# Kernel optimization log

Hardware: AMD Instinct MI355X
Metric: run time of the kernel (lower is better)

Reference implementation:

```python
import jax, jax.numpy as jnp
import numpy as np
from jax import lax

KS = 3
N = KS * KS  # 9 sampling points per output pixel


def conv2d(x, w, b, stride=1, pad=1):
    out = lax.conv_general_dilated(
        x, w, (stride, stride), [(pad, pad), (pad, pad)],
        dimension_numbers=("NCHW", "OIHW", "NCHW"))
    return out + b[None, :, None, None]


def setup_inputs() -> dict:
    key = jax.random.key(0)
    k1, k2, k3, k4, k5 = jax.random.split(key, 5)
    inc, outc, b, h, w = 64, 128, 8, 128, 128
    x = jax.random.normal(k1, (b, inc, h, w), jnp.float32)
    # offsets conv: inc -> 3*ks*ks channels, 3x3, pad 1 (small init so offsets are modest)
    off_w = jax.random.normal(k2, (3 * N, inc, 3, 3), jnp.float32) * 0.01
    off_b = jax.random.normal(k3, (3 * N,), jnp.float32) * 0.01
    # main conv: inc -> outc, 3x3, stride=ks, pad 1
    conv_w = jax.random.normal(k4, (outc, inc, 3, 3), jnp.float32) * (1.0 / np.sqrt(inc * 9))
    conv_b = jax.random.normal(k5, (outc,), jnp.float32) * 0.01
    return {"x": x, "off_w": off_w, "off_b": off_b, "conv_w": conv_w, "conv_b": conv_b}


def _deform_forward(x, off_w, off_b, conv_w, conv_b):
    b, c, h, w = x.shape
    ow = conv2d(x, off_w, off_b)               # (b, 3N, h, w)
    offset = ow[:, :2 * N]                      # offset_x (N) then offset_y (N); 3rd chunk (sigmoid
                                                # modulation) is computed in torch but never used.
    # p_0: integer grid coordinates, broadcast over N sampling points
    ii = jnp.arange(h, dtype=x.dtype)
    jj = jnp.arange(w, dtype=x.dtype)
    p0x = jnp.broadcast_to(ii[None, None, :, None], (1, N, h, w))
    p0y = jnp.broadcast_to(jj[None, None, None, :], (1, N, h, w))
    p0 = jnp.concatenate([p0x, p0y], axis=1)    # (1, 2N, h, w)
    p = (p0 + offset).transpose(0, 2, 3, 1)     # (b, h, w, 2N)
    px, py = p[..., :N], p[..., N:]

    q = jnp.floor(p)                            # detached in torch; floor grad is 0 anyway
    qltx = jnp.clip(q[..., :N], 0, h - 1).astype(jnp.int32)
    qlty = jnp.clip(q[..., N:], 0, w - 1).astype(jnp.int32)
    qrbx = jnp.clip(q[..., :N] + 1, 0, h - 1).astype(jnp.int32)
    qrby = jnp.clip(q[..., N:] + 1, 0, w - 1).astype(jnp.int32)

    pxc = jnp.clip(px, 0, h - 1)
    pyc = jnp.clip(py, 0, w - 1)

    xf = x.reshape(b, c, h * w)

    def gather(qx, qy):
        idx = (qx * w + qy).reshape(b, -1)      # (b, h*w*N)
        g = jax.vmap(lambda xb, ib: xb[:, ib])(xf, idx)  # (b, c, h*w*N)
        return g.reshape(b, c, h, w, N)

    f = lambda q_: q_.astype(x.dtype)
    g_lt = (1 + (f(qltx) - pxc)) * (1 + (f(qlty) - pyc))
    g_rb = (1 - (f(qrbx) - pxc)) * (1 - (f(qrby) - pyc))
    g_lb = (1 + (f(qltx) - pxc)) * (1 - (f(qrby) - pyc))
    g_rt = (1 - (f(qrbx) - pxc)) * (1 + (f(qlty) - pyc))

    xo = (g_lt[:, None] * gather(qltx, qlty)
          + g_rb[:, None] * gather(qrbx, qrby)
          + g_lb[:, None] * gather(qltx, qrby)
          + g_rt[:, None] * gather(qrbx, qlty))  # (b, c, h, w, N)

    # rearrange: b c h w (kr kc) -> b c (h kr) (w kc)
    xo = xo.reshape(b, c, h, w, KS, KS).transpose(0, 1, 2, 4, 3, 5).reshape(b, c, h * KS, w * KS)
    return conv2d(xo, conv_w, conv_b, stride=KS, pad=1)  # (b, outc, h, w)


def reference(x, off_w, off_b, conv_w, conv_b):
    return _deform_forward(x, off_w, off_b, conv_w, conv_b)
```

## Files before the change

### kernel.cpp

```cpp
#include <hip/hip_runtime.h>
#include <hip/hip_fp16.h>

#define BB   8
#define CC   64
#define HH   128
#define WW   128
#define OCC  128
#define HWx  (HH*WW)
#define KTOT 576
#define SST  584

typedef __attribute__((ext_vector_type(8))) short short8t;
typedef __attribute__((ext_vector_type(8))) _Float16 half8t;
typedef __attribute__((ext_vector_type(4))) float f32x4;

static __device__ __forceinline__ ushort f2h(float f) {
    __half h = __float2half_rn(f);
    return __half_as_ushort(h);
}

__global__ __launch_bounds__(256) void kfront2(const float* __restrict__ x,
                                               ushort* __restrict__ xTh,
                                               ushort* __restrict__ xTl,
                                               const float* __restrict__ cw,
                                               ushort* __restrict__ wf,
                                               const float* __restrict__ ow,
                                               ushort* __restrict__ woh,
                                               ushort* __restrict__ wol) {
    int bi  = blockIdx.x;
    int tid = threadIdx.x;

    if (bi < 2048) {
        int bb = bi;
        int b  = bb >> 8;
        int p  = (bb & 255) * 64 + (tid & 63);
        int cg = tid >> 6;
        const float* xb = x + (size_t)b * CC * HWx + p;
        size_t base = ((size_t)b * HWx + p) * 64 + cg * 16;
        short8t h0, h1, l0, l1;
#pragma unroll
        for (int e = 0; e < 8; ++e) {
            float v = xb[(size_t)(cg * 16 + e) * HWx];
            __half h = __float2half_rn(v);
            h0[e] = (short)__half_as_ushort(h);
            l0[e] = (short)f2h((v - __half2float(h)) * 2048.f);
        }
#pragma unroll
        for (int e = 0; e < 8; ++e) {
            float v = xb[(size_t)(cg * 16 + 8 + e) * HWx];
            __half h = __float2half_rn(v);
            h1[e] = (short)__half_as_ushort(h);
            l1[e] = (short)f2h((v - __half2float(h)) * 2048.f);
        }
        *(short8t*)(xTh + base)     = h0;
        *(short8t*)(xTh + base + 8) = h1;
        *(short8t*)(xTl + base)     = l0;
        *(short8t*)(xTl + base + 8) = l1;

    } else if (bi < 2336) {
        int i = (bi - 2048) * 256 + tid;
        int e  = i & 7;
        int t  = i >> 3;
        int l  = t & 63;
        int t2 = t >> 6;
        int lr = l & 15, lg = l >> 4;
        int oc = (t2 / 18) * 16 + lr;
        int kg = (t2 % 18) * 32 + lg * 8 + e;
        int c = kg & 63, tap = kg >> 6;
        wf[i] = f2h(cw[oc * 576 + c * 9 + tap]);

    } else {
        int idx = (bi - 2336) * 256 + tid;
        int t   = idx / 18432;
        int r   = idx - t * 18432;
        int nt  = r / 9216;
        int r2  = r - nt * 9216;
        int ks  = r2 / 512;
        int r3  = r2 - ks * 512;
        int l   = r3 >> 3;
        int e   = r3 & 7;
        int k   = ks * 32 + (l >> 4) * 8 + e;
        int tap = k >> 6, c = k & 63;
        int ch  = nt * 16 + (l & 15);
        float val = (ch < 18) ? ow[ch * 576 + c * 9 + tap] * 1024.f : 0.f;
        __half h = __float2half_rn(val);
        if (t == 0) woh[r] = __half_as_ushort(h);
        else        wol[r] = f2h(val - __half2float(h));
    }
}

__global__ __launch_bounds__(256) void koffM(const ushort* __restrict__ xTh,
                                             const ushort* __restrict__ xTl,
                                             const ushort* __restrict__ woh,
                                             const ushort* __restrict__ wol,
                                             const float* __restrict__ off_b,
                                             float* __restrict__ offsT) {
    int tid = threadIdx.x;
    int bi  = blockIdx.x;
    int b   = bi & 7;
    int i   = bi >> 3;
    int wv  = tid >> 6;
    int l   = tid & 63;
    int lr  = l & 15, lg = l >> 4;
    const ushort* xh = xTh + (size_t)b * HWx * 64;
    const ushort* xl = xTl + (size_t)b * HWx * 64;

    f32x4 accA[2][2], accB[2][2];
#pragma unroll
    for (int mt = 0; mt < 2; ++mt)
#pragma unroll
        for (int nt = 0; nt < 2; ++nt)
#pragma unroll
            for (int e = 0; e < 4; ++e) { accA[mt][nt][e] = 0.f; accB[mt][nt][e] = 0.f; }

#pragma unroll
    for (int ks = 0; ks < 18; ++ks) {
        int tap = ks >> 1;
        int di = tap / 3, dj = tap - di * 3;
        int si = i + di - 1;
        bool sv = (si >= 0) && (si < HH);
        int c0 = (ks & 1) * 32 + lg * 8;

        half8t Bh0 = *(const half8t*)(woh + ((0 * 18 + ks) * 64 + l) * 8);
        half8t Bl0 = *(const half8t*)(wol + ((0 * 18 + ks) * 64 + l) * 8);
        half8t Bh1 = *(const half8t*)(woh + ((1 * 18 + ks) * 64 + l) * 8);
        half8t Bl1 = *(const half8t*)(wol + ((1 * 18 + ks) * 64 + l) * 8);

#pragma unroll
        for (int mt = 0; mt < 2; ++mt) {
            int j  = wv * 32 + mt * 16 + lr;
            int sj = j + dj - 1;
            bool v = sv && (sj >= 0) && (sj < WW);
            half8t Ah = {0, 0, 0, 0, 0, 0, 0, 0};
            half8t Al = {0, 0, 0, 0, 0, 0, 0, 0};
            if (v) {
                size_t ao = ((size_t)(si * WW + sj)) * 64 + c0;
                Ah = *(const half8t*)(xh + ao);
                Al = *(const half8t*)(xl + ao);
            }
            accA[mt][0] = __builtin_amdgcn_mfma_f32_16x16x32_f16(Ah, Bh0, accA[mt][0], 0, 0, 0);
            accA[mt][0] = __builtin_amdgcn_mfma_f32_16x16x32_f16(Ah, Bl0, accA[mt][0], 0, 0, 0);
            accB[mt][0] = __builtin_amdgcn_mfma_f32_16x16x32_f16(Al, Bh0, accB[mt][0], 0, 0, 0);
            accA[mt][1] = __builtin_amdgcn_mfma_f32_16x16x32_f16(Ah, Bh1, accA[mt][1], 0, 0, 0);
            accA[mt][1] = __builtin_amdgcn_mfma_f32_16x16x32_f16(Ah, Bl1, accA[mt][1], 0, 0, 0);
            accB[mt][1] = __builtin_amdgcn_mfma_f32_16x16x32_f16(Al, Bh1, accB[mt][1], 0, 0, 0);
        }
    }

    const float sA = 1.f / 1024.f;
    const float sB = 1.f / (1024.f * 2048.f);
#pragma unroll
    for (int mt = 0; mt < 2; ++mt)
#pragma unroll
        for (int nt = 0; nt < 2; ++nt) {
            int ch = nt * 16 + lr;
            if (ch < 18) {
                float bv = off_b[ch];
#pragma unroll
                for (int e = 0; e < 4; ++e) {
                    int pix = wv * 32 + mt * 16 + lg * 4 + e;
                    float val = accA[mt][nt][e] * sA + accB[mt][nt][e] * sB + bv;
                    offsT[((size_t)(b * HWx) + i * WW + pix) * 18 + ch] = val;
                }
            }
        }
}

static __device__ __forceinline__ __half2 lerp_w(uint ltw, uint rbw, uint lbw, uint rtw,
                                                 __half2 hlt, __half2 hrb,
                                                 __half2 hlb, __half2 hrt) {
    __half2 a;
    a = __hmul2(hlt, __builtin_bit_cast(__half2, ltw));
    a = __hfma2(hrb, __builtin_bit_cast(__half2, rbw), a);
    a = __hfma2(hlb, __builtin_bit_cast(__half2, lbw), a);
    a = __hfma2(hrt, __builtin_bit_cast(__half2, rtw), a);
    return a;
}
static __device__ __forceinline__ uint4 lerp_u4(uint4 lt, uint4 rb, uint4 lb, uint4 rt,
                                                __half2 hlt, __half2 hrb,
                                                __half2 hlb, __half2 hrt) {
    uint4 o;
    o.x = __builtin_bit_cast(uint, lerp_w(lt.x, rb.x, lb.x, rt.x, hlt, hrb, hlb, hrt));
    o.y = __builtin_bit_cast(uint, lerp_w(lt.y, rb.y, lb.y, rt.y, hlt, hrb, hlb, hrt));
    o.z = __builtin_bit_cast(uint, lerp_w(lt.z, rb.z, lb.z, rt.z, hlt, hrb, hlb, hrt));
    o.w = __builtin_bit_cast(uint, lerp_w(lt.w, rb.w, lb.w, rt.w, hlt, hrb, hlb, hrt));
    return o;
}

__global__ __launch_bounds__(512, 4) void kmain23(const ushort* __restrict__ xT,
                                                  const float* __restrict__ offsT,
                                                  const ushort* __restrict__ wf,
                                                  const float* __restrict__ conv_b,
                                                  float* __restrict__ out) {
    __shared__ __align__(16) ushort S[32 * SST];
    int tid = threadIdx.x;
    int bi  = blockIdx.x;
    int b   = bi & 7;
    int rem = bi >> 3;
    int oi  = rem >> 2;
    int oj0 = (rem & 3) * 32;

    const ushort* xTb  = xT + (size_t)b * HWx * 64;
    const float*  offb = offsT + (size_t)b * HWx * 18;

    int wv = tid >> 6;
    int l  = tid & 63;
    int lr = l & 15;
    int lg = l >> 4;
    const ushort* wr0 = wf + ((size_t)(wv * 18) * 64 + l) * 8;

#pragma unroll
    for (int it = 0; it < 3; ++it) {
        int s = tid + it * 512;
        if (s >= 1152) break;
        int pix = s / 36;
        int rr  = s - pix * 36;
        int tap = rr >> 2;
        int cg2 = rr & 3;
        int kr = tap / 3, kc = tap - kr * 3;
        int si = oi + ((kr == 0) ? -1 : 0);
        int sj = oj0 + pix + ((kc == 0) ? -1 : 0);
        ushort* Sd = &S[pix * SST + tap * 64 + cg2 * 16];

        if (si < 0 || sj < 0) {
            uint4 z = {0, 0, 0, 0};
            *(uint4*)Sd = z;
            *(uint4*)(Sd + 8) = z;
            continue;
        }
        int n    = ((kr == 0) ? 2 : kr - 1) * 3 + ((kc == 0) ? 2 : kc - 1);
        int pidx = si * WW + sj;
        float ox = offb[pidx * 18 + n];
        float oy = offb[pidx * 18 + 9 + n];
        float px = (float)si + ox;
        float py = (float)sj + oy;
        float fx = floorf(px), fy = floorf(py);
        float pxc   = fminf(fmaxf(px, 0.f), 127.f);
        float pyc   = fminf(fmaxf(py, 0.f), 127.f);
        float qltxf = fminf(fmaxf(fx, 0.f), 127.f);
        float qltyf = fminf(fmaxf(fy, 0.f), 127.f);
        float qrbxf = fminf(fmaxf(fx + 1.f, 0.f), 127.f);
        float qrbyf = fminf(fmaxf(fy + 1.f, 0.f), 127.f);
        int qltx = (int)qltxf, qlty = (int)qltyf;
        int qrbx = (int)qrbxf, qrby = (int)qrbyf;
        int co = cg2 * 16;
        const ushort* plt = xTb + (size_t)(qltx * WW + qlty) * 64 + co;
        const ushort* prb = xTb + (size_t)(qrbx * WW + qrby) * 64 + co;
        const ushort* plb = xTb + (size_t)(qltx * WW + qrby) * 64 + co;
        const ushort* prt = xTb + (size_t)(qrbx * WW + qlty) * 64 + co;
        uint4 lt0 = *(const uint4*)(plt);  uint4 lt1 = *(const uint4*)(plt + 8);
        uint4 rb0 = *(const uint4*)(prb);  uint4 rb1 = *(const uint4*)(prb + 8);
        uint4 lb0 = *(const uint4*)(plb);  uint4 lb1 = *(const uint4*)(plb + 8);
        uint4 rt0 = *(const uint4*)(prt);  uint4 rt1 = *(const uint4*)(prt + 8);

        float glt = (1.f + (qltxf - pxc)) * (1.f + (qltyf - pyc));
        float grb = (1.f - (qrbxf - pxc)) * (1.f - (qrbyf - pyc));
        float glb = (1.f + (qltxf - pxc)) * (1.f - (qrbyf - pyc));
        float grt = (1.f - (qrbxf - pxc)) * (1.f + (qltyf - pyc));
        __half2 hlt = __float2half2_rn(glt);
        __half2 hrb = __float2half2_rn(grb);
        __half2 hlb = __float2half2_rn(glb);
        __half2 hrt = __float2half2_rn(grt);

        uint4 o0 = lerp_u4(lt0, rb0, lb0, rt0, hlt, hrb, hlb, hrt);
        uint4 o1 = lerp_u4(lt1, rb1, lb1, rt1, hlt, hrb, hlb, hrt);
        *(uint4*)(Sd)     = o0;
        *(uint4*)(Sd + 8) = o1;
    }
    __syncthreads();

    f32x4 acc[2];
#pragma unroll
    for (int e = 0; e < 4; ++e) {
        float bv = conv_b[16 * wv + lg * 4 + e];
        acc[0][e] = bv;
        acc[1][e] = bv;
    }
    const ushort* s0 = &S[(lr) * SST + lg * 8];
    const ushort* s1 = &S[(16 + lr) * SST + lg * 8];

#pragma unroll
    for (int ks = 0; ks < 18; ++ks) {
        int kk = ks * 32;
        half8t a0 = *(const half8t*)(wr0 + ks * 512);
        half8t b0 = *(const half8t*)(s0 + kk);
        half8t b1 = *(const half8t*)(s1 + kk);
        acc[0] = __builtin_amdgcn_mfma_f32_16x16x32_f16(a0, b0, acc[0], 0, 0, 0);
        acc[1] = __builtin_amdgcn_mfma_f32_16x16x32_f16(a0, b1, acc[1], 0, 0, 0);
    }

    float* ob = out + ((size_t)b * OCC * HH + oi) * WW + oj0;
#pragma unroll
    for (int p = 0; p < 2; ++p) {
#pragma unroll
        for (int e = 0; e < 4; ++e) {
            int oc  = 16 * wv + lg * 4 + e;
            int col = 16 * p + lr;
            ob[(size_t)oc * HWx + col] = acc[p][e];
        }
    }
}

extern "C" void kernel_launch(void* const* d_in, const int* in_sizes, int n_in,
                              void* d_out, int out_size, void* d_ws, size_t ws_size,
                              hipStream_t stream) {
    const float* x      = (const float*)d_in[0];
    const float* off_w  = (const float*)d_in[1];
    const float* off_b  = (const float*)d_in[2];
    const float* conv_w = (const float*)d_in[3];
    const float* conv_b = (const float*)d_in[4];
    float* out = (float*)d_out;

    char* w0 = (char*)d_ws;
    ushort* wbf   = (ushort*)w0;
    float*  offsT = (float*)(w0 + 147456);
    ushort* xTh   = (ushort*)(w0 + 147456 + 9437184);
    ushort* xTl   = (ushort*)(w0 + 147456 + 9437184 + 16777216);
    ushort* woh   = (ushort*)(w0 + 147456 + 9437184 + 2 * 16777216);
    ushort* wol   = (ushort*)(w0 + 147456 + 9437184 + 2 * 16777216 + 36864);

    kfront2<<<2480, 256, 0, stream>>>(x, xTh, xTl, conv_w, wbf, off_w, woh, wol);
    koffM<<<BB * HH, 256, 0, stream>>>(xTh, xTl, woh, wol, off_b, offsT);
    kmain23<<<BB * HH * 4, 512, 0, stream>>>(xTh, offsT, wbf, conv_b, out);
}
```

Measured before the change: 112.5 us.

## Fuse offset conv into front kernel reading fp32 input directly

The offset convolution now reads the fp32 NCHW input directly and does the hi/lo fp16 split in registers, instead of reading a precomputed transposed xTh/xTl pair. It runs inside the same launch as the xTh transpose and the weight prep. The xTl buffer and its write traffic are removed, and the offset-weight prep moves to a small kernel that runs first. In exchange, the offset conv now does strided, channel-major fp32 loads (eight separate loads per fragment, each a full plane apart) that are less coalesced than the earlier 16-byte vector loads.

```diff
diff --git a/kernel.cpp b/kernel.cpp
--- a/kernel.cpp
+++ b/kernel.cpp
@@ -19,46 +19,128 @@
     return __half_as_ushort(h);
 }
 
-__global__ __launch_bounds__(256) void kfront2(const float* __restrict__ x,
-                                               ushort* __restrict__ xTh,
-                                               ushort* __restrict__ xTl,
-                                               const float* __restrict__ cw,
-                                               ushort* __restrict__ wf,
-                                               const float* __restrict__ ow,
+__global__ __launch_bounds__(256) void kprepw2(const float* __restrict__ ow,
                                                ushort* __restrict__ woh,
                                                ushort* __restrict__ wol) {
+    int idx = blockIdx.x * 256 + threadIdx.x;
+    int t   = idx / 18432;
+    int r   = idx - t * 18432;
+    int nt  = r / 9216;
+    int r2  = r - nt * 9216;
+    int ks  = r2 / 512;
+    int r3  = r2 - ks * 512;
+    int l   = r3 >> 3;
+    int e   = r3 & 7;
+    int k   = ks * 32 + (l >> 4) * 8 + e;
+    int tap = k >> 6, c = k & 63;
+    int ch  = nt * 16 + (l & 15);
+    float val = (ch < 18) ? ow[ch * 576 + c * 9 + tap] * 1024.f : 0.f;
+    __half h = __float2half_rn(val);
+    if (t == 0) woh[r] = __half_as_ushort(h);
+    else        wol[r] = f2h(val - __half2float(h));
+}
+
+__global__ __launch_bounds__(256) void kfront3(const float* __restrict__ x,
+                                               const ushort* __restrict__ woh,
+                                               const ushort* __restrict__ wol,
+                                               const float* __restrict__ off_b,
+                                               float* __restrict__ offsT,
+                                               ushort* __restrict__ xTh,
+                                               const float* __restrict__ cw,
+                                               ushort* __restrict__ wf) {
     int bi  = blockIdx.x;
     int tid = threadIdx.x;
 
-    if (bi < 2048) {
-        int bb = bi;
+    if (bi < 1024) {
+        int b = bi & 7;
+        int i = bi >> 3;
+        int wv = tid >> 6;
+        int l  = tid & 63;
+        int lr = l & 15, lg = l >> 4;
+        const float* xb = x + (size_t)b * CC * HWx;
+
+        f32x4 accA[2][2], accB[2][2];
+#pragma unroll
+        for (int mt = 0; mt < 2; ++mt)
+#pragma unroll
+            for (int nt = 0; nt < 2; ++nt)
+#pragma unroll
+                for (int e = 0; e < 4; ++e) { accA[mt][nt][e] = 0.f; accB[mt][nt][e] = 0.f; }
+
+#pragma unroll
+        for (int ks = 0; ks < 18; ++ks) {
+            int tap = ks >> 1;
+            int di = tap / 3, dj = tap - di * 3;
+            int si = i + di - 1;
+            bool sv = (si >= 0) && (si < HH);
+            int c0 = (ks & 1) * 32 + lg * 8;
+
+            half8t Bh0 = *(const half8t*)(woh + ((0 * 18 + ks) * 64 + l) * 8);
+            half8t Bl0 = *(const half8t*)(wol + ((0 * 18 + ks) * 64 + l) * 8);
+            half8t Bh1 = *(const half8t*)(woh + ((1 * 18 + ks) * 64 + l) * 8);
+            half8t Bl1 = *(const half8t*)(wol + ((1 * 18 + ks) * 64 + l) * 8);
+
+#pragma unroll
+            for (int mt = 0; mt < 2; ++mt) {
+                int j  = wv * 32 + mt * 16 + lr;
+                int sj = j + dj - 1;
+                bool v = sv && (sj >= 0) && (sj < WW);
+                half8t Ah = {0, 0, 0, 0, 0, 0, 0, 0};
+                half8t Al = {0, 0, 0, 0, 0, 0, 0, 0};
+                if (v) {
+                    const float* xp = xb + (size_t)c0 * HWx + si * WW + sj;
+#pragma unroll
+                    for (int e = 0; e < 8; ++e) {
+                        float val = xp[(size_t)e * HWx];
+                        _Float16 h = (_Float16)val;
+                        Ah[e] = h;
+                        Al[e] = (_Float16)((val - (float)h) * 2048.f);
+                    }
+                }
+                accA[mt][0] = __builtin_amdgcn_mfma_f32_16x16x32_f16(Ah, Bh0, accA[mt][0], 0, 0, 0);
+                accA[mt][0] = __builtin_amdgcn_mfma_f32_16x16x32_f16(Ah, Bl0, accA[mt][0], 0, 0, 0);
+                accB[mt][0] = __builtin_amdgcn_mfma_f32_16x16x32_f16(Al, Bh0, accB[mt][0], 0, 0, 0);
+                accA[mt][1] = __builtin_amdgcn_mfma_f32_16x16x32_f16(Ah, Bh1, accA[mt][1], 0, 0, 0);
+                accA[mt][1] = __builtin_amdgcn_mfma_f32_16x16x32_f16(Ah, Bl1, accA[mt][1], 0, 0, 0);
+                accB[mt][1] = __builtin_amdgcn_mfma_f32_16x16x32_f16(Al, Bh1, accB[mt][1], 0, 0, 0);
+            }
+        }
+
+        const float sA = 1.f / 1024.f;
+        const float sB = 1.f / (1024.f * 2048.f);
+#pragma unroll
+        for (int mt = 0; mt < 2; ++mt)
+#pragma unroll
+            for (int nt = 0; nt < 2; ++nt) {
+                int ch = nt * 16 + lr;
+                if (ch < 18) {
+                    float bv = off_b[ch];
+#pragma unroll
+                    for (int e = 0; e < 4; ++e) {
+                        int pix = wv * 32 + mt * 16 + lg * 4 + e;
+                        float val = accA[mt][nt][e] * sA + accB[mt][nt][e] * sB + bv;
+                        offsT[((size_t)(b * HWx) + i * WW + pix) * 18 + ch] = val;
+                    }
+                }
+            }
+
+    } else if (bi < 3072) {
+        int bb = bi - 1024;
         int b  = bb >> 8;
         int p  = (bb & 255) * 64 + (tid & 63);
         int cg = tid >> 6;
         const float* xb = x + (size_t)b * CC * HWx + p;
-        size_t base = ((size_t)b * HWx + p) * 64 + cg * 16;
-        short8t h0, h1, l0, l1;
-#pragma unroll
-        for (int e = 0; e < 8; ++e) {
-            float v = xb[(size_t)(cg * 16 + e) * HWx];
-            __half h = __float2half_rn(v);
-            h0[e] = (short)__half_as_ushort(h);
-            l0[e] = (short)f2h((v - __half2float(h)) * 2048.f);
-        }
-#pragma unroll
-        for (int e = 0; e < 8; ++e) {
-            float v = xb[(size_t)(cg * 16 + 8 + e) * HWx];
-            __half h = __float2half_rn(v);
-            h1[e] = (short)__half_as_ushort(h);
-            l1[e] = (short)f2h((v - __half2float(h)) * 2048.f);
-        }
-        *(short8t*)(xTh + base)     = h0;
-        *(short8t*)(xTh + base + 8) = h1;
-        *(short8t*)(xTl + base)     = l0;
-        *(short8t*)(xTl + base + 8) = l1;
-
-    } else if (bi < 2336) {
-        int i = (bi - 2048) * 256 + tid;
+        ushort* ob = xTh + ((size_t)b * HWx + p) * 64 + cg * 16;
+        short8t v0, v1;
+#pragma unroll
+        for (int e = 0; e < 8; ++e) v0[e] = (short)f2h(xb[(size_t)(cg * 16 + e) * HWx]);
+#pragma unroll
+        for (int e = 0; e < 8; ++e) v1[e] = (short)f2h(xb[(size_t)(cg * 16 + 8 + e) * HWx]);
+        *(short8t*)ob = v0;
+        *(short8t*)(ob + 8) = v1;
+
+    } else {
+        int i = (bi - 3072) * 256 + tid;
         int e  = i & 7;
         int t  = i >> 3;
         int l  = t & 63;
@@ -68,102 +150,7 @@
         int kg = (t2 % 18) * 32 + lg * 8 + e;
         int c = kg & 63, tap = kg >> 6;
         wf[i] = f2h(cw[oc * 576 + c * 9 + tap]);
-
-    } else {
-        int idx = (bi - 2336) * 256 + tid;
-        int t   = idx / 18432;
-        int r   = idx - t * 18432;
-        int nt  = r / 9216;
-        int r2  = r - nt * 9216;
-        int ks  = r2 / 512;
-        int r3  = r2 - ks * 512;
-        int l   = r3 >> 3;
-        int e   = r3 & 7;
-        int k   = ks * 32 + (l >> 4) * 8 + e;
-        int tap = k >> 6, c = k & 63;
-        int ch  = nt * 16 + (l & 15);
-        float val = (ch < 18) ? ow[ch * 576 + c * 9 + tap] * 1024.f : 0.f;
-        __half h = __float2half_rn(val);
-        if (t == 0) woh[r] = __half_as_ushort(h);
-        else        wol[r] = f2h(val - __half2float(h));
-    }
-}
-
-__global__ __launch_bounds__(256) void koffM(const ushort* __restrict__ xTh,
-                                             const ushort* __restrict__ xTl,
-                                             const ushort* __restrict__ woh,
-                                             const ushort* __restrict__ wol,
-                                             const float* __restrict__ off_b,
-                                             float* __restrict__ offsT) {
-    int tid = threadIdx.x;
-    int bi  = blockIdx.x;
-    int b   = bi & 7;
-    int i   = bi >> 3;
-    int wv  = tid >> 6;
-    int l   = tid & 63;
-    int lr  = l & 15, lg = l >> 4;
-    const ushort* xh = xTh + (size_t)b * HWx * 64;
-    const ushort* xl = xTl + (size_t)b * HWx * 64;
-
-    f32x4 accA[2][2], accB[2][2];
-#pragma unroll
-    for (int mt = 0; mt < 2; ++mt)
-#pragma unroll
-        for (int nt = 0; nt < 2; ++nt)
-#pragma unroll
-            for (int e = 0; e < 4; ++e) { accA[mt][nt][e] = 0.f; accB[mt][nt][e] = 0.f; }
-
-#pragma unroll
-    for (int ks = 0; ks < 18; ++ks) {
-        int tap = ks >> 1;
-        int di = tap / 3, dj = tap - di * 3;
-        int si = i + di - 1;
-        bool sv = (si >= 0) && (si < HH);
-        int c0 = (ks & 1) * 32 + lg * 8;
-
-        half8t Bh0 = *(const half8t*)(woh + ((0 * 18 + ks) * 64 + l) * 8);
-        half8t Bl0 = *(const half8t*)(wol + ((0 * 18 + ks) * 64 + l) * 8);
-        half8t Bh1 = *(const half8t*)(woh + ((1 * 18 + ks) * 64 + l) * 8);
-        half8t Bl1 = *(const half8t*)(wol + ((1 * 18 + ks) * 64 + l) * 8);
-
-#pragma unroll
-        for (int mt = 0; mt < 2; ++mt) {
-            int j  = wv * 32 + mt * 16 + lr;
-            int sj = j + dj - 1;
-            bool v = sv && (sj >= 0) && (sj < WW);
-            half8t Ah = {0, 0, 0, 0, 0, 0, 0, 0};
-            half8t Al = {0, 0, 0, 0, 0, 0, 0, 0};
-            if (v) {
-                size_t ao = ((size_t)(si * WW + sj)) * 64 + c0;
-                Ah = *(const half8t*)(xh + ao);
-                Al = *(const half8t*)(xl + ao);
-            }
-            accA[mt][0] = __builtin_amdgcn_mfma_f32_16x16x32_f16(Ah, Bh0, accA[mt][0], 0, 0, 0);
-            accA[mt][0] = __builtin_amdgcn_mfma_f32_16x16x32_f16(Ah, Bl0, accA[mt][0], 0, 0, 0);
-            accB[mt][0] = __builtin_amdgcn_mfma_f32_16x16x32_f16(Al, Bh0, accB[mt][0], 0, 0, 0);
-            accA[mt][1] = __builtin_amdgcn_mfma_f32_16x16x32_f16(Ah, Bh1, accA[mt][1], 0, 0, 0);
-            accA[mt][1] = __builtin_amdgcn_mfma_f32_16x16x32_f16(Ah, Bl1, accA[mt][1], 0, 0, 0);
-            accB[mt][1] = __builtin_amdgcn_mfma_f32_16x16x32_f16(Al, Bh1, accB[mt][1], 0, 0, 0);
-        }
-    }
-
-    const float sA = 1.f / 1024.f;
-    const float sB = 1.f / (1024.f * 2048.f);
-#pragma unroll
-    for (int mt = 0; mt < 2; ++mt)
-#pragma unroll
-        for (int nt = 0; nt < 2; ++nt) {
-            int ch = nt * 16 + lr;
-            if (ch < 18) {
-                float bv = off_b[ch];
-#pragma unroll
-                for (int e = 0; e < 4; ++e) {
-                    int pix = wv * 32 + mt * 16 + lg * 4 + e;
-                    float val = accA[mt][nt][e] * sA + accB[mt][nt][e] * sB + bv;
-                    offsT[((size_t)(b * HWx) + i * WW + pix) * 18 + ch] = val;
-                }
-            }
-        }
+    }
 }
 
 static __device__ __forceinline__ __half2 lerp_w(uint ltw, uint rbw, uint lbw, uint rtw,
@@ -187,7 +174,7 @@
     return o;
 }
 
-__global__ __launch_bounds__(512, 4) void kmain23(const ushort* __restrict__ xT,
+__global__ __launch_bounds__(512, 4) void kmain24(const ushort* __restrict__ xT,
                                                   const float* __restrict__ offsT,
                                                   const ushort* __restrict__ wf,
                                                   const float* __restrict__ conv_b,
@@ -315,11 +302,10 @@
     ushort* wbf   = (ushort*)w0;
     float*  offsT = (float*)(w0 + 147456);
     ushort* xTh   = (ushort*)(w0 + 147456 + 9437184);
-    ushort* xTl   = (ushort*)(w0 + 147456 + 9437184 + 16777216);
-    ushort* woh   = (ushort*)(w0 + 147456 + 9437184 + 2 * 16777216);
-    ushort* wol   = (ushort*)(w0 + 147456 + 9437184 + 2 * 16777216 + 36864);
-
-    kfront2<<<2480, 256, 0, stream>>>(x, xTh, xTl, conv_w, wbf, off_w, woh, wol);
-    koffM<<<BB * HH, 256, 0, stream>>>(xTh, xTl, woh, wol, off_b, offsT);
-    kmain23<<<BB * HH * 4, 512, 0, stream>>>(xTh, offsT, wbf, conv_b, out);
-}
+    ushort* woh   = (ushort*)(w0 + 147456 + 9437184 + 16777216);
+    ushort* wol   = (ushort*)(w0 + 147456 + 9437184 + 16777216 + 36864);
+
+    kprepw2<<<144, 256, 0, stream>>>(off_w, woh, wol);
+    kfront3<<<3360, 256, 0, stream>>>(x, woh, wol, off_b, offsT, xTh, conv_w, wbf);
+    kmain24<<<BB * HH * 4, 512, 0, stream>>>(xTh, offsT, wbf, conv_b, out);
+}
```

After: 95.65 us. 14.9% less time.
